# Optimization experiments

Measured on AMD Instinct MI355X. Metric: run time of the kernel, lower is better.

## Reference

```python
import jax, jax.numpy as jnp
import numpy as np

DIM = 256
TIME_DIM = 64
BETA = 0.5
VOCAB = 150
B, L = 2048, 128


def setup_inputs() -> dict:
    key = jax.random.key(0)
    ks = jax.random.split(key, 9)
    u = lambda k, shape: jax.random.uniform(k, shape, jnp.float32, -0.1, 0.1)
    return {
        "out": jax.random.normal(ks[0], (B, L, DIM), jnp.float32),
        "hn": jax.random.normal(ks[1], (B, DIM), jnp.float32),
        "pos_ind": jax.random.randint(ks[2], (B, L), 0, VOCAB),
        "rel_dt": jax.random.randint(ks[3], (B, L), 0, VOCAB),
        "abs_dt": jnp.zeros((B, L), jnp.float32),
        "pos_emb_w": u(ks[4], (VOCAB, TIME_DIM)),
        "rel_emb_w": u(ks[5], (VOCAB, TIME_DIM)),
        "Wk": u(ks[6], (DIM, DIM)),   # fc_k.weight: y = x @ Wk.T
        "Wq": u(ks[7], (DIM, DIM)),   # fc_q.weight
        "Wrp": u(ks[8], (1, 2 * TIME_DIM)),  # fc_rp.weight
    }


def reference(out, hn, pos_ind, rel_dt, abs_dt, pos_emb_w, rel_emb_w, Wk, Wq, Wrp):
    temperature = np.sqrt(DIM * 1.0).astype(np.float32)
    pad_mask = pos_ind == 0                      # [B, L]
    pos_e = pos_emb_w[pos_ind]                   # [B, L, T]
    rel_e = rel_emb_w[rel_dt]                    # [B, L, T]
    attn_k = jnp.einsum('bld,ed->ble', out, Wk)  # fc_k(out)
    attn_q = jnp.einsum('bd,ed->be', hn, Wq)     # fc_q(hn)
    attn_0 = jnp.einsum('bld,bd->bl', attn_k, attn_q) / temperature
    attn_1 = jnp.einsum('blt,ot->bl', jnp.concatenate([rel_e, pos_e], -1), Wrp)
    attn = attn_0 + BETA * attn_1
    attn = jnp.where(pad_mask, -jnp.inf, attn)
    attn = jax.nn.softmax(attn, axis=1)
    return jnp.einsum('bl,bld->bd', attn, out)   # [B, D]
```

## Files before the change

kernel.cpp:

```cpp
#include <hip/hip_runtime.h>

#define DIM 256
#define L_ 128
#define TD 64
#define NVOCAB 150
#define NB 2048

__global__ __launch_bounds__(256) void prep_kernel(
    const float* __restrict__ Wk, const float* __restrict__ Wq,
    const float* __restrict__ Wrp,
    const float* __restrict__ rel_emb_w, const float* __restrict__ pos_emb_w,
    float* __restrict__ M, float* __restrict__ rel_s, float* __restrict__ pos_s)
{
    if (blockIdx.x == DIM) {
        int v = threadIdx.x;
        if (v < NVOCAB) {
            float sr = 0.f, sp = 0.f;
            for (int j = 0; j < TD; ++j) {
                sr = fmaf(rel_emb_w[v * TD + j], Wrp[j], sr);
                sp = fmaf(pos_emb_w[v * TD + j], Wrp[TD + j], sp);
            }
            rel_s[v] = 0.5f * sr;
            pos_s[v] = 0.5f * sp;
        }
        return;
    }
    int c = blockIdx.x;
    int d = threadIdx.x;
    float acc = 0.f;
    for (int e = 0; e < DIM; ++e)
        acc = fmaf(Wq[e * DIM + c], Wk[e * DIM + d], acc);
    M[c * DIM + d] = acc * (1.0f / 16.0f);
}

__global__ __launch_bounds__(256) void qk_kernel(
    const float* __restrict__ hn, const float* __restrict__ M,
    float* __restrict__ qk)
{
    __shared__ float hn_s[8][DIM];
    const int r0 = blockIdx.x * 8;
    const int t = threadIdx.x;
#pragma unroll
    for (int i = 0; i < 8; ++i)
        hn_s[i][t] = hn[(size_t)(r0 + i) * DIM + t];
    __syncthreads();
    float acc[8] = {0.f, 0.f, 0.f, 0.f, 0.f, 0.f, 0.f, 0.f};
    for (int c = 0; c < DIM; ++c) {
        float m = M[c * DIM + t];
#pragma unroll
        for (int r = 0; r < 8; ++r)
            acc[r] = fmaf(hn_s[r][c], m, acc[r]);
    }
#pragma unroll
    for (int r = 0; r < 8; ++r)
        qk[(size_t)(r0 + r) * DIM + t] = acc[r];
}

__global__ __launch_bounds__(512, 4) void attn_main(
    const float* __restrict__ outp, const float* __restrict__ qk,
    const int* __restrict__ pos_ind, const int* __restrict__ rel_dt,
    const float* __restrict__ rel_s, const float* __restrict__ pos_s,
    float* __restrict__ y)
{
    const int b = blockIdx.x;
    const int t = threadIdx.x;
    const int w = t >> 6;
    const int lane = t & 63;

    __shared__ float logits[L_];
    __shared__ float bias[L_];
    __shared__ float red[8][DIM];
    __shared__ float ms[2];

    const float4 q4 = *reinterpret_cast<const float4*>(qk + (size_t)b * DIM + lane * 4);

    if (t < L_) {
        int pi = pos_ind[(size_t)b * L_ + t];
        int rd = rel_dt[(size_t)b * L_ + t];
        bias[t] = (pi == 0) ? -1e30f : (rel_s[rd] + pos_s[pi]);
    }

    const float4* src = reinterpret_cast<const float4*>(outp + (size_t)b * (L_ * DIM));
    float4 v[16];
    float p[16];
#pragma unroll
    for (int k = 0; k < 16; ++k) {
        v[k] = src[k * 512 + t];
        p[k] = v[k].x * q4.x + v[k].y * q4.y + v[k].z * q4.z + v[k].w * q4.w;
    }
#pragma unroll
    for (int k = 0; k < 16; ++k) {
#pragma unroll
        for (int off = 32; off > 0; off >>= 1)
            p[k] += __shfl_xor(p[k], off, 64);
    }
    if (lane == 0) {
#pragma unroll
        for (int k = 0; k < 16; ++k)
            logits[k * 8 + w] = p[k];
    }
    __syncthreads();
    if (t < L_) logits[t] += bias[t];
    __syncthreads();

    if (w == 0) {
        float a = logits[lane];
        float c2 = logits[lane + 64];
        float mx = fmaxf(a, c2);
#pragma unroll
        for (int off = 32; off > 0; off >>= 1)
            mx = fmaxf(mx, __shfl_xor(mx, off, 64));
        float s = __expf(a - mx) + __expf(c2 - mx);
#pragma unroll
        for (int off = 32; off > 0; off >>= 1)
            s += __shfl_xor(s, off, 64);
        if (lane == 0) { ms[0] = mx; ms[1] = 1.0f / s; }
    }
    __syncthreads();
    const float mx = ms[0], inv_s = ms[1];
    if (t < L_) logits[t] = __expf(logits[t] - mx) * inv_s;
    __syncthreads();

    float o0 = 0.f, o1 = 0.f, o2 = 0.f, o3 = 0.f;
#pragma unroll
    for (int k = 0; k < 16; ++k) {
        float wk = logits[k * 8 + w];
        o0 = fmaf(wk, v[k].x, o0);
        o1 = fmaf(wk, v[k].y, o1);
        o2 = fmaf(wk, v[k].z, o2);
        o3 = fmaf(wk, v[k].w, o3);
    }
    *reinterpret_cast<float4*>(&red[w][lane * 4]) = make_float4(o0, o1, o2, o3);
    __syncthreads();

    if (t < DIM) {
        float s = 0.f;
#pragma unroll
        for (int ww = 0; ww < 8; ++ww)
            s += red[ww][t];
        y[(size_t)b * DIM + t] = s;
    }
}

extern "C" void kernel_launch(void* const* d_in, const int* in_sizes, int n_in,
                              void* d_out, int out_size, void* d_ws, size_t ws_size,
                              hipStream_t stream)
{
    const float* out_t     = (const float*)d_in[0];
    const float* hn        = (const float*)d_in[1];
    const int*   pos_ind   = (const int*)  d_in[2];
    const int*   rel_dt    = (const int*)  d_in[3];
    const float* pos_emb_w = (const float*)d_in[5];
    const float* rel_emb_w = (const float*)d_in[6];
    const float* Wk        = (const float*)d_in[7];
    const float* Wq        = (const float*)d_in[8];
    const float* Wrp       = (const float*)d_in[9];

    float* y = (float*)d_out;

    float* M     = (float*)d_ws;
    float* qk    = M + DIM * DIM;
    float* rel_s = qk + (size_t)NB * DIM;
    float* pos_s = rel_s + 256;

    prep_kernel<<<DIM + 1, 256, 0, stream>>>(Wk, Wq, Wrp, rel_emb_w, pos_emb_w,
                                             M, rel_s, pos_s);
    qk_kernel<<<NB / 8, 256, 0, stream>>>(hn, M, qk);
    attn_main<<<NB, 512, 0, stream>>>(out_t, qk, pos_ind, rel_dt, rel_s, pos_s, y);
}
```

Before: 83.08 us.

## Use online softmax with 16-lane row groups and precompute bias in qk kernel

Reworks the attention kernel so each 16-lane group handles whole rows. The dot product needs only a 4-step shuffle, and an online (flash-style) softmax accumulates the weighted output as rows stream in, with two register sets alternating to overlap the next loads. This removes the separate logits/max/sum passes and several barriers. The pad/bias computation moves into extra blocks of the qk kernel and is written to global memory. The trade-off is a larger shared reduction buffer (32x256 floats), which may lower occupancy, plus the extra exp and rescale work in the online update.

```diff
diff --git a/kernel.cpp b/kernel.cpp
--- a/kernel.cpp
+++ b/kernel.cpp
@@ -25,21 +25,30 @@
         }
         return;
     }
-    int c = blockIdx.x;
-    int d = threadIdx.x;
+    int cc = blockIdx.x;
+    int d  = threadIdx.x;
     float acc = 0.f;
     for (int e = 0; e < DIM; ++e)
-        acc = fmaf(Wq[e * DIM + c], Wk[e * DIM + d], acc);
-    M[c * DIM + d] = acc * (1.0f / 16.0f);
+        acc = fmaf(Wq[e * DIM + cc], Wk[e * DIM + d], acc);
+    M[cc * DIM + d] = acc * (1.0f / 16.0f);
 }
 
-__global__ __launch_bounds__(256) void qk_kernel(
+__global__ __launch_bounds__(256) void qk_bias_kernel(
     const float* __restrict__ hn, const float* __restrict__ M,
-    float* __restrict__ qk)
+    const int* __restrict__ pos_ind, const int* __restrict__ rel_dt,
+    const float* __restrict__ rel_s, const float* __restrict__ pos_s,
+    float* __restrict__ qk, float* __restrict__ bias_g)
 {
+    const int t = threadIdx.x;
+    if (blockIdx.x >= NB / 8) {
+        int idx = (blockIdx.x - NB / 8) * 256 + t;
+        int pi = pos_ind[idx];
+        int rd = rel_dt[idx];
+        bias_g[idx] = (pi == 0) ? -1e30f : (rel_s[rd] + pos_s[pi]);
+        return;
+    }
     __shared__ float hn_s[8][DIM];
     const int r0 = blockIdx.x * 8;
-    const int t = threadIdx.x;
 #pragma unroll
     for (int i = 0; i < 8; ++i)
         hn_s[i][t] = hn[(size_t)(r0 + i) * DIM + t];
@@ -56,88 +65,94 @@
         qk[(size_t)(r0 + r) * DIM + t] = acc[r];
 }
 
+__device__ __forceinline__ float dot4(float4 a, float4 b) {
+    return fmaf(a.x, b.x, fmaf(a.y, b.y, fmaf(a.z, b.z, a.w * b.w)));
+}
+
 __global__ __launch_bounds__(512, 4) void attn_main(
     const float* __restrict__ outp, const float* __restrict__ qk,
-    const int* __restrict__ pos_ind, const int* __restrict__ rel_dt,
-    const float* __restrict__ rel_s, const float* __restrict__ pos_s,
-    float* __restrict__ y)
+    const float* __restrict__ bias_g, float* __restrict__ y)
 {
-    const int b = blockIdx.x;
-    const int t = threadIdx.x;
-    const int w = t >> 6;
+    const int b    = blockIdx.x;
+    const int t    = threadIdx.x;
+    const int w    = t >> 6;
     const int lane = t & 63;
+    const int g    = lane >> 4;
+    const int c    = lane & 15;
+    const int grp  = (w << 2) | g;
 
-    __shared__ float logits[L_];
-    __shared__ float bias[L_];
-    __shared__ float red[8][DIM];
-    __shared__ float ms[2];
+    __shared__ float mG[32];
+    __shared__ float dG[32];
+    __shared__ float red[32][DIM];
 
-    const float4 q4 = *reinterpret_cast<const float4*>(qk + (size_t)b * DIM + lane * 4);
+    const float4* __restrict__ src = (const float4*)outp + (size_t)b * (L_ * 64);
+    const int r0   = (w << 4) | g;
+    const int base = r0 * 64 + c;
 
-    if (t < L_) {
-        int pi = pos_ind[(size_t)b * L_ + t];
-        int rd = rel_dt[(size_t)b * L_ + t];
-        bias[t] = (pi == 0) ? -1e30f : (rel_s[rd] + pos_s[pi]);
-    }
+    float4 X0 = src[base +   0], X1 = src[base +  16], X2 = src[base +  32], X3 = src[base +  48];
+    float4 Y0 = src[base + 256], Y1 = src[base + 272], Y2 = src[base + 288], Y3 = src[base + 304];
 
-    const float4* src = reinterpret_cast<const float4*>(outp + (size_t)b * (L_ * DIM));
-    float4 v[16];
-    float p[16];
-#pragma unroll
-    for (int k = 0; k < 16; ++k) {
-        v[k] = src[k * 512 + t];
-        p[k] = v[k].x * q4.x + v[k].y * q4.y + v[k].z * q4.z + v[k].w * q4.w;
-    }
-#pragma unroll
-    for (int k = 0; k < 16; ++k) {
-#pragma unroll
-        for (int off = 32; off > 0; off >>= 1)
-            p[k] += __shfl_xor(p[k], off, 64);
-    }
-    if (lane == 0) {
-#pragma unroll
-        for (int k = 0; k < 16; ++k)
-            logits[k * 8 + w] = p[k];
-    }
-    __syncthreads();
-    if (t < L_) logits[t] += bias[t];
+    const float4* __restrict__ qp = (const float4*)qk + (size_t)b * 64;
+    const float4 q0 = qp[c], q1 = qp[c + 16], q2 = qp[c + 32], q3 = qp[c + 48];
+
+    const float* __restrict__ bp = bias_g + (size_t)b * L_ + r0;
+    const float bi0 = bp[0], bi1 = bp[4], bi2 = bp[8], bi3 = bp[12];
+
+    float m = -1e30f, d = 0.f;
+    float4 o0 = {0,0,0,0}, o1 = {0,0,0,0}, o2 = {0,0,0,0}, o3 = {0,0,0,0};
+
+#define PROC(A0, A1, A2, A3, BI) do {                                        \
+        float p = dot4(A0, q0) + dot4(A1, q1) + dot4(A2, q2) + dot4(A3, q3); \
+        p += __shfl_xor(p, 1);                                               \
+        p += __shfl_xor(p, 2);                                               \
+        p += __shfl_xor(p, 4);                                               \
+        p += __shfl_xor(p, 8);                                               \
+        float logit = p + (BI);                                              \
+        float mn = fmaxf(m, logit);                                          \
+        float sc = __expf(m - mn);                                           \
+        float we = __expf(logit - mn);                                       \
+        d = d * sc + we;                                                     \
+        m = mn;                                                              \
+        o0.x = fmaf(we, A0.x, o0.x * sc); o0.y = fmaf(we, A0.y, o0.y * sc);  \
+        o0.z = fmaf(we, A0.z, o0.z * sc); o0.w = fmaf(we, A0.w, o0.w * sc);  \
+        o1.x = fmaf(we, A1.x, o1.x * sc); o1.y = fmaf(we, A1.y, o1.y * sc);  \
+        o1.z = fmaf(we, A1.z, o1.z * sc); o1.w = fmaf(we, A1.w, o1.w * sc);  \
+        o2.x = fmaf(we, A2.x, o2.x * sc); o2.y = fmaf(we, A2.y, o2.y * sc);  \
+        o2.z = fmaf(we, A2.z, o2.z * sc); o2.w = fmaf(we, A2.w, o2.w * sc);  \
+        o3.x = fmaf(we, A3.x, o3.x * sc); o3.y = fmaf(we, A3.y, o3.y * sc);  \
+        o3.z = fmaf(we, A3.z, o3.z * sc); o3.w = fmaf(we, A3.w, o3.w * sc);  \
+    } while (0)
+
+    PROC(X0, X1, X2, X3, bi0);
+    X0 = src[base + 512]; X1 = src[base + 528]; X2 = src[base + 544]; X3 = src[base + 560];
+    PROC(Y0, Y1, Y2, Y3, bi1);
+    Y0 = src[base + 768]; Y1 = src[base + 784]; Y2 = src[base + 800]; Y3 = src[base + 816];
+    PROC(X0, X1, X2, X3, bi2);
+    PROC(Y0, Y1, Y2, Y3, bi3);
+#undef PROC
+
+    if (c == 0) { mG[grp] = m; dG[grp] = d; }
     __syncthreads();
 
-    if (w == 0) {
-        float a = logits[lane];
-        float c2 = logits[lane + 64];
-        float mx = fmaxf(a, c2);
+    float M2 = -1e30f;
 #pragma unroll
-        for (int off = 32; off > 0; off >>= 1)
-            mx = fmaxf(mx, __shfl_xor(mx, off, 64));
-        float s = __expf(a - mx) + __expf(c2 - mx);
+    for (int i = 0; i < 32; ++i) M2 = fmaxf(M2, mG[i]);
+    float D = 0.f;
 #pragma unroll
-        for (int off = 32; off > 0; off >>= 1)
-            s += __shfl_xor(s, off, 64);
-        if (lane == 0) { ms[0] = mx; ms[1] = 1.0f / s; }
-    }
-    __syncthreads();
-    const float mx = ms[0], inv_s = ms[1];
-    if (t < L_) logits[t] = __expf(logits[t] - mx) * inv_s;
-    __syncthreads();
+    for (int i = 0; i < 32; ++i) D += __expf(mG[i] - M2) * dG[i];
+    const float f = __expf(m - M2) / D;
 
-    float o0 = 0.f, o1 = 0.f, o2 = 0.f, o3 = 0.f;
-#pragma unroll
-    for (int k = 0; k < 16; ++k) {
-        float wk = logits[k * 8 + w];
-        o0 = fmaf(wk, v[k].x, o0);
-        o1 = fmaf(wk, v[k].y, o1);
-        o2 = fmaf(wk, v[k].z, o2);
-        o3 = fmaf(wk, v[k].w, o3);
-    }
-    *reinterpret_cast<float4*>(&red[w][lane * 4]) = make_float4(o0, o1, o2, o3);
+    float4* rw = (float4*)(&red[grp][0]);
+    rw[c]      = make_float4(o0.x * f, o0.y * f, o0.z * f, o0.w * f);
+    rw[c + 16] = make_float4(o1.x * f, o1.y * f, o1.z * f, o1.w * f);
+    rw[c + 32] = make_float4(o2.x * f, o2.y * f, o2.z * f, o2.w * f);
+    rw[c + 48] = make_float4(o3.x * f, o3.y * f, o3.z * f, o3.w * f);
     __syncthreads();
 
     if (t < DIM) {
         float s = 0.f;
 #pragma unroll
-        for (int ww = 0; ww < 8; ++ww)
-            s += red[ww][t];
+        for (int gg = 0; gg < 32; ++gg) s += red[gg][t];
         y[(size_t)b * DIM + t] = s;
     }
 }
@@ -158,13 +173,15 @@
 
     float* y = (float*)d_out;
 
-    float* M     = (float*)d_ws;
-    float* qk    = M + DIM * DIM;
-    float* rel_s = qk + (size_t)NB * DIM;
-    float* pos_s = rel_s + 256;
+    float* M      = (float*)d_ws;
+    float* qk     = M + DIM * DIM;
+    float* rel_s  = qk + (size_t)NB * DIM;
+    float* pos_s  = rel_s + 256;
+    float* bias_g = pos_s + 256;
 
     prep_kernel<<<DIM + 1, 256, 0, stream>>>(Wk, Wq, Wrp, rel_emb_w, pos_emb_w,
                                              M, rel_s, pos_s);
-    qk_kernel<<<NB / 8, 256, 0, stream>>>(hn, M, qk);
-    attn_main<<<NB, 512, 0, stream>>>(out_t, qk, pos_ind, rel_dt, rel_s, pos_s, y);
+    qk_bias_kernel<<<NB / 8 + (NB * L_) / 256, 256, 0, stream>>>(
+        hn, M, pos_ind, rel_dt, rel_s, pos_s, qk, bias_g);
+    attn_main<<<NB, 512, 0, stream>>>(out_t, qk, bias_g, y);
 }
```

After: 78.51 us. 5.5% less time.

## Split attention over sequence into four partial blocks with flash-style combine pass

Applied to the files above, without the earlier changes.

Replaces the one-block-per-batch attention kernel with a split-L scheme. Each of four blocks handles 32 rows and produces a partial output plus a local max and denominator, and a second kernel merges them with online-softmax rescaling. The aim is more parallelism and shorter per-block critical paths, so memory latency is hidden better when streaming the 256MB `out` tensor. The cost is an extra launch and a round trip of the partial outputs (about 8MB) through global memory. Unroll pragmas are also added to the prep and qk loops.

```diff
diff --git a/kernel.cpp b/kernel.cpp
--- a/kernel.cpp
+++ b/kernel.cpp
@@ -5,6 +5,10 @@
 #define TD 64
 #define NVOCAB 150
 #define NB 2048
+
+__device__ __forceinline__ float dot4(float4 a, float4 b) {
+    return fmaf(a.x, b.x, fmaf(a.y, b.y, fmaf(a.z, b.z, a.w * b.w)));
+}
 
 __global__ __launch_bounds__(256) void prep_kernel(
     const float* __restrict__ Wk, const float* __restrict__ Wq,
@@ -16,6 +20,7 @@
         int v = threadIdx.x;
         if (v < NVOCAB) {
             float sr = 0.f, sp = 0.f;
+#pragma unroll 8
             for (int j = 0; j < TD; ++j) {
                 sr = fmaf(rel_emb_w[v * TD + j], Wrp[j], sr);
                 sp = fmaf(pos_emb_w[v * TD + j], Wrp[TD + j], sp);
@@ -25,12 +30,13 @@
         }
         return;
     }
-    int c = blockIdx.x;
-    int d = threadIdx.x;
+    int cc = blockIdx.x;
+    int d  = threadIdx.x;
     float acc = 0.f;
+#pragma unroll 16
     for (int e = 0; e < DIM; ++e)
-        acc = fmaf(Wq[e * DIM + c], Wk[e * DIM + d], acc);
-    M[c * DIM + d] = acc * (1.0f / 16.0f);
+        acc = fmaf(Wq[e * DIM + cc], Wk[e * DIM + d], acc);
+    M[cc * DIM + d] = acc * (1.0f / 16.0f);
 }
 
 __global__ __launch_bounds__(256) void qk_kernel(
@@ -45,6 +51,7 @@
         hn_s[i][t] = hn[(size_t)(r0 + i) * DIM + t];
     __syncthreads();
     float acc[8] = {0.f, 0.f, 0.f, 0.f, 0.f, 0.f, 0.f, 0.f};
+#pragma unroll 8
     for (int c = 0; c < DIM; ++c) {
         float m = M[c * DIM + t];
 #pragma unroll
@@ -56,90 +63,104 @@
         qk[(size_t)(r0 + r) * DIM + t] = acc[r];
 }
 
-__global__ __launch_bounds__(512, 4) void attn_main(
+__global__ __launch_bounds__(256, 5) void attn_pass1(
     const float* __restrict__ outp, const float* __restrict__ qk,
     const int* __restrict__ pos_ind, const int* __restrict__ rel_dt,
     const float* __restrict__ rel_s, const float* __restrict__ pos_s,
+    float* __restrict__ part_o, float* __restrict__ part_md)
+{
+    const int pb  = blockIdx.x;
+    const int b   = pb >> 2;
+    const int h   = pb & 3;
+    const int t   = threadIdx.x;
+    const int grp = t >> 4;
+    const int c   = t & 15;
+
+    __shared__ float mG[16];
+    __shared__ float dG[16];
+    __shared__ float red[16][DIM];
+
+    const float4* __restrict__ src = (const float4*)outp + (size_t)b * (L_ * 64);
+    const int r0 = h * 32 + grp;
+    float4 v0[4], v1[4];
+#pragma unroll
+    for (int j = 0; j < 4; ++j) v0[j] = src[(r0     ) * 64 + j * 16 + c];
+#pragma unroll
+    for (int j = 0; j < 4; ++j) v1[j] = src[(r0 + 16) * 64 + j * 16 + c];
+
+    const float4* __restrict__ qp = (const float4*)qk + (size_t)b * 64;
+    float4 q[4];
+#pragma unroll
+    for (int j = 0; j < 4; ++j) q[j] = qp[j * 16 + c];
+
+    const int pi0 = pos_ind[b * L_ + r0],      rd0 = rel_dt[b * L_ + r0];
+    const int pi1 = pos_ind[b * L_ + r0 + 16], rd1 = rel_dt[b * L_ + r0 + 16];
+    const float bi0 = (pi0 == 0) ? -1e30f : (rel_s[rd0] + pos_s[pi0]);
+    const float bi1 = (pi1 == 0) ? -1e30f : (rel_s[rd1] + pos_s[pi1]);
+
+    float p0 = dot4(v0[0], q[0]) + dot4(v0[1], q[1]) + dot4(v0[2], q[2]) + dot4(v0[3], q[3]);
+    float p1 = dot4(v1[0], q[0]) + dot4(v1[1], q[1]) + dot4(v1[2], q[2]) + dot4(v1[3], q[3]);
+    p0 += __shfl_xor(p0, 1);  p1 += __shfl_xor(p1, 1);
+    p0 += __shfl_xor(p0, 2);  p1 += __shfl_xor(p1, 2);
+    p0 += __shfl_xor(p0, 4);  p1 += __shfl_xor(p1, 4);
+    p0 += __shfl_xor(p0, 8);  p1 += __shfl_xor(p1, 8);
+    const float lg0 = p0 + bi0, lg1 = p1 + bi1;
+
+    const float m  = fmaxf(lg0, lg1);
+    const float w0 = __expf(lg0 - m), w1 = __expf(lg1 - m);
+    const float d  = w0 + w1;
+
+    if (c == 0) { mG[grp] = m; dG[grp] = d; }
+    __syncthreads();
+    float Mb = mG[0];
+#pragma unroll
+    for (int g = 1; g < 16; ++g) Mb = fmaxf(Mb, mG[g]);
+    const float f   = __expf(m - Mb);
+    const float fw0 = f * w0, fw1 = f * w1;
+    if (t == 0) {
+        float D = 0.f;
+#pragma unroll
+        for (int g = 0; g < 16; ++g) D += dG[g] * __expf(mG[g] - Mb);
+        part_md[pb * 2]     = Mb;
+        part_md[pb * 2 + 1] = D;
+    }
+    float4* rw = (float4*)(&red[grp][0]);
+#pragma unroll
+    for (int j = 0; j < 4; ++j) {
+        float4 o;
+        o.x = fmaf(fw0, v0[j].x, fw1 * v1[j].x);
+        o.y = fmaf(fw0, v0[j].y, fw1 * v1[j].y);
+        o.z = fmaf(fw0, v0[j].z, fw1 * v1[j].z);
+        o.w = fmaf(fw0, v0[j].w, fw1 * v1[j].w);
+        rw[j * 16 + c] = o;
+    }
+    __syncthreads();
+
+    float s = 0.f;
+#pragma unroll
+    for (int g = 0; g < 16; ++g) s += red[g][t];
+    part_o[(size_t)pb * DIM + t] = s;
+}
+
+__global__ __launch_bounds__(256) void attn_pass2(
+    const float* __restrict__ part_o, const float* __restrict__ part_md,
     float* __restrict__ y)
 {
     const int b = blockIdx.x;
     const int t = threadIdx.x;
-    const int w = t >> 6;
-    const int lane = t & 63;
-
-    __shared__ float logits[L_];
-    __shared__ float bias[L_];
-    __shared__ float red[8][DIM];
-    __shared__ float ms[2];
-
-    const float4 q4 = *reinterpret_cast<const float4*>(qk + (size_t)b * DIM + lane * 4);
-
-    if (t < L_) {
-        int pi = pos_ind[(size_t)b * L_ + t];
-        int rd = rel_dt[(size_t)b * L_ + t];
-        bias[t] = (pi == 0) ? -1e30f : (rel_s[rd] + pos_s[pi]);
-    }
-
-    const float4* src = reinterpret_cast<const float4*>(outp + (size_t)b * (L_ * DIM));
-    float4 v[16];
-    float p[16];
-#pragma unroll
-    for (int k = 0; k < 16; ++k) {
-        v[k] = src[k * 512 + t];
-        p[k] = v[k].x * q4.x + v[k].y * q4.y + v[k].z * q4.z + v[k].w * q4.w;
-    }
-#pragma unroll
-    for (int k = 0; k < 16; ++k) {
-#pragma unroll
-        for (int off = 32; off > 0; off >>= 1)
-            p[k] += __shfl_xor(p[k], off, 64);
-    }
-    if (lane == 0) {
-#pragma unroll
-        for (int k = 0; k < 16; ++k)
-            logits[k * 8 + w] = p[k];
-    }
-    __syncthreads();
-    if (t < L_) logits[t] += bias[t];
-    __syncthreads();
-
-    if (w == 0) {
-        float a = logits[lane];
-        float c2 = logits[lane + 64];
-        float mx = fmaxf(a, c2);
-#pragma unroll
-        for (int off = 32; off > 0; off >>= 1)
-            mx = fmaxf(mx, __shfl_xor(mx, off, 64));
-        float s = __expf(a - mx) + __expf(c2 - mx);
-#pragma unroll
-        for (int off = 32; off > 0; off >>= 1)
-            s += __shfl_xor(s, off, 64);
-        if (lane == 0) { ms[0] = mx; ms[1] = 1.0f / s; }
-    }
-    __syncthreads();
-    const float mx = ms[0], inv_s = ms[1];
-    if (t < L_) logits[t] = __expf(logits[t] - mx) * inv_s;
-    __syncthreads();
-
-    float o0 = 0.f, o1 = 0.f, o2 = 0.f, o3 = 0.f;
-#pragma unroll
-    for (int k = 0; k < 16; ++k) {
-        float wk = logits[k * 8 + w];
-        o0 = fmaf(wk, v[k].x, o0);
-        o1 = fmaf(wk, v[k].y, o1);
-        o2 = fmaf(wk, v[k].z, o2);
-        o3 = fmaf(wk, v[k].w, o3);
-    }
-    *reinterpret_cast<float4*>(&red[w][lane * 4]) = make_float4(o0, o1, o2, o3);
-    __syncthreads();
-
-    if (t < DIM) {
-        float s = 0.f;
-#pragma unroll
-        for (int ww = 0; ww < 8; ++ww)
-            s += red[ww][t];
-        y[(size_t)b * DIM + t] = s;
-    }
+    const float m0 = part_md[(b * 4 + 0) * 2], e0 = part_md[(b * 4 + 0) * 2 + 1];
+    const float m1 = part_md[(b * 4 + 1) * 2], e1 = part_md[(b * 4 + 1) * 2 + 1];
+    const float m2 = part_md[(b * 4 + 2) * 2], e2 = part_md[(b * 4 + 2) * 2 + 1];
+    const float m3 = part_md[(b * 4 + 3) * 2], e3 = part_md[(b * 4 + 3) * 2 + 1];
+    const float Mx = fmaxf(fmaxf(m0, m1), fmaxf(m2, m3));
+    const float w0 = __expf(m0 - Mx), w1 = __expf(m1 - Mx);
+    const float w2 = __expf(m2 - Mx), w3 = __expf(m3 - Mx);
+    const float D  = e0 * w0 + e1 * w1 + e2 * w2 + e3 * w3;
+    float s = part_o[(size_t)(b * 4 + 0) * DIM + t] * w0;
+    s = fmaf(part_o[(size_t)(b * 4 + 1) * DIM + t], w1, s);
+    s = fmaf(part_o[(size_t)(b * 4 + 2) * DIM + t], w2, s);
+    s = fmaf(part_o[(size_t)(b * 4 + 3) * DIM + t], w3, s);
+    y[(size_t)b * DIM + t] = s / D;
 }
 
 extern "C" void kernel_launch(void* const* d_in, const int* in_sizes, int n_in,
@@ -158,13 +179,17 @@
 
     float* y = (float*)d_out;
 
-    float* M     = (float*)d_ws;
-    float* qk    = M + DIM * DIM;
-    float* rel_s = qk + (size_t)NB * DIM;
-    float* pos_s = rel_s + 256;
+    float* M       = (float*)d_ws;
+    float* qk      = M + DIM * DIM;
+    float* rel_s   = qk + (size_t)NB * DIM;
+    float* pos_s   = rel_s + 256;
+    float* part_o  = pos_s + 256;
+    float* part_md = part_o + (size_t)NB * 4 * DIM;
 
     prep_kernel<<<DIM + 1, 256, 0, stream>>>(Wk, Wq, Wrp, rel_emb_w, pos_emb_w,
                                              M, rel_s, pos_s);
     qk_kernel<<<NB / 8, 256, 0, stream>>>(hn, M, qk);
-    attn_main<<<NB, 512, 0, stream>>>(out_t, qk, pos_ind, rel_dt, rel_s, pos_s, y);
+    attn_pass1<<<NB * 4, 256, 0, stream>>>(out_t, qk, pos_ind, rel_dt,
+                                           rel_s, pos_s, part_o, part_md);
+    attn_pass2<<<NB, 256, 0, stream>>>(part_o, part_md, y);
 }
```

Measured after the change: 76.52 us. 1.09x faster.
